# Optimization experiments

Measured on AMD Instinct MI355X. Metric: run time of the kernel, lower is better.

The kernel has to match this reference:

```python
import jax, jax.numpy as jnp
import numpy as np

DIM = 512
HEADS = 8
WS = 8  # window_size


def setup_inputs() -> dict:
    key = jax.random.key(0)
    ks = jax.random.split(key, 7)
    b, c, h, w = 4, DIM, 192, 192
    x = jax.random.normal(ks[0], (b, c, h, w), dtype=jnp.float32)
    # conv1x1 weights are [out, in] matrices (kernel dim squeezed)
    wq = jax.random.normal(ks[1], (DIM, DIM), dtype=jnp.float32) * 0.02
    wk = jax.random.normal(ks[2], (DIM, DIM), dtype=jnp.float32) * 0.02
    wv = jax.random.normal(ks[3], (DIM, DIM), dtype=jnp.float32) * 0.02
    wo = jax.random.normal(ks[4], (DIM, DIM), dtype=jnp.float32) * 0.02
    bo = jax.random.normal(ks[5], (DIM,), dtype=jnp.float32) * 0.02
    # learned per-head additive bias over window tokens (trunc_normal std=0.02)
    beta = jax.random.normal(ks[6], (HEADS, WS * WS, WS * WS), dtype=jnp.float32) * 0.02
    return {"x": x, "wq": wq, "wk": wk, "wv": wv, "wo": wo, "bo": bo, "beta": beta}


def reference(x, wq, wk, wv, wo, bo, beta):
    b, c, h, w = x.shape
    s = WS
    pad_r = (-w) % s
    pad_b = (-h) % s
    x = jnp.pad(x, ((0, 0), (0, 0), (0, pad_b), (0, pad_r)))
    H, W = h + pad_b, w + pad_r
    nh, nw = H // s, W // s
    n = s * s
    head_dim = c // HEADS
    scale = head_dim ** -0.5
    # window partition: (b, c, nh, s, nw, s) -> (b*nh*nw, c, n)
    xw = x.reshape(b, c, nh, s, nw, s).transpose(0, 2, 4, 1, 3, 5).reshape(b * nh * nw, c, n)
    B = xw.shape[0]
    q = jnp.einsum('oc,bcn->bon', wq, xw).reshape(B, HEADS, head_dim, n)
    k = jnp.einsum('oc,bcn->bon', wk, xw).reshape(B, HEADS, head_dim, n)
    v = jnp.einsum('oc,bcn->bon', wv, xw).reshape(B, HEADS, head_dim, n)
    attn = jnp.einsum('bhdn,bhdm->bhnm', q, k) * scale + beta  # [B,H,n,n]
    attn = jax.nn.softmax(attn, axis=-1)
    o = jnp.einsum('bhnm,bhdm->bhdn', attn, v).reshape(B, c, n)
    o = jnp.einsum('oc,bcn->bon', wo, o) + bo[None, :, None]
    # window merge back to image
    out = o.reshape(b, nh, nw, c, s, s).transpose(0, 3, 1, 4, 2, 5).reshape(b, c, H, W)
    return out[:, :, :h, :w]
```

## Files before the change

kernel.cpp:

```cpp
#include <hip/hip_runtime.h>

typedef unsigned short ushort_t;
typedef __attribute__((ext_vector_type(4))) float f32x4;
typedef __attribute__((ext_vector_type(8))) short short8;

__device__ __forceinline__ ushort_t f2bf(float f) {
  union { float f; unsigned u; } v; v.f = f;
  unsigned r = v.u + 0x7fffu + ((v.u >> 16) & 1u);
  return (ushort_t)(r >> 16);
}
__device__ __forceinline__ unsigned pack2(float lo, float hi) {
  return (unsigned)f2bf(lo) | ((unsigned)f2bf(hi) << 16);
}

__global__ __launch_bounds__(256) void cvt_w_k(const float* __restrict__ wq,
                                               const float* __restrict__ wk,
                                               const float* __restrict__ wv,
                                               const float* __restrict__ wo,
                                               ushort_t* __restrict__ dst) {
  int idx = (blockIdx.x * 256 + threadIdx.x) * 4;
  int m = idx >> 18;
  int off = idx & 0x3ffff;
  const float* s = (m == 0) ? wq : (m == 1) ? wk : (m == 2) ? wv : wo;
  float4 v = *(const float4*)(s + off);
  ushort4 o;
  o.x = f2bf(v.x); o.y = f2bf(v.y); o.z = f2bf(v.z); o.w = f2bf(v.w);
  *(ushort4*)(dst + idx) = o;
}

__global__ __launch_bounds__(256) void xpose_k(const float* __restrict__ x,
                                               ushort_t* __restrict__ xT) {
  __shared__ ushort_t tile[128 * 80];
  int bid = blockIdx.x;
  int win = bid >> 2, kc = bid & 3;
  int b = win / 576, rem = win % 576, wh = rem / 24, ww = rem % 24;
  int tid = threadIdx.x;
  {
    int c_l = tid >> 1, half = tid & 1;
    const float* xb = x + ((((size_t)b * 512 + kc * 128 + c_l) * 192 + wh * 8) * 192 + ww * 8);
#pragma unroll
    for (int ii = 0; ii < 4; ++ii) {
      int i = half * 4 + ii;
      float4 v0 = *(const float4*)(xb + i * 192);
      float4 v1 = *(const float4*)(xb + i * 192 + 4);
      uint4 u;
      u.x = (unsigned)f2bf(v0.x) | ((unsigned)f2bf(v0.y) << 16);
      u.y = (unsigned)f2bf(v0.z) | ((unsigned)f2bf(v0.w) << 16);
      u.z = (unsigned)f2bf(v1.x) | ((unsigned)f2bf(v1.y) << 16);
      u.w = (unsigned)f2bf(v1.z) | ((unsigned)f2bf(v1.w) << 16);
      *(uint4*)&tile[c_l * 80 + i * 8] = u;
    }
  }
  __syncthreads();
  {
    int tok = tid >> 2, q = tid & 3;
    unsigned w[16];
#pragma unroll
    for (int k = 0; k < 16; ++k) {
      unsigned lo = tile[(q * 32 + 2 * k) * 80 + tok];
      unsigned hi = tile[(q * 32 + 2 * k + 1) * 80 + tok];
      w[k] = lo | (hi << 16);
    }
    ushort_t* d = xT + ((size_t)(win * 64 + tok) * 512 + kc * 128 + q * 32);
#pragma unroll
    for (int s2 = 0; s2 < 4; ++s2) {
      uint4 u; u.x = w[s2 * 4 + 0]; u.y = w[s2 * 4 + 1]; u.z = w[s2 * 4 + 2]; u.w = w[s2 * 4 + 3];
      *(uint4*)(d + s2 * 8) = u;
    }
  }
}

__global__ __launch_bounds__(512, 2) void qkv_attn5_k(const ushort_t* __restrict__ xT,
                                                      const ushort_t* __restrict__ wB,
                                                      const float* __restrict__ beta,
                                                      ushort_t* __restrict__ O) {
  __shared__ __align__(16) ushort_t smem[2 * 8704 + 2 * 4608 + 2 * 4608];
  ushort_t* xstage = smem;
  ushort_t* qs = smem + 17408;
  ushort_t* ks = smem + 26624;
  ushort_t* vs = smem;

  int win = blockIdx.x;
  int t0 = win * 64;
  int tid = threadIdx.x, lane = tid & 63, wid = tid >> 6;
  int l15 = lane & 15, l4 = lane >> 4;

  int srow[2], sslot[2];
#pragma unroll
  for (int c = 0; c < 2; ++c) { int u = c * 512 + tid; srow[c] = u >> 4; sslot[c] = u & 15; }

  const f32x4 z = {0.f, 0.f, 0.f, 0.f};

  for (int hcc = 0; hcc < 4; ++hcc) {
    f32x4 aq[4], ak[4], av[4];
#pragma unroll
    for (int i = 0; i < 4; ++i) { aq[i] = z; ak[i] = z; av[i] = z; }
    int ocol = hcc * 128 + wid * 16 + l15;
    const ushort_t* wqr = wB + (size_t)ocol * 512 + l4 * 8;
    const ushort_t* wkr = wqr + 262144;
    const ushort_t* wvr = wqr + 524288;

#pragma unroll
    for (int c = 0; c < 2; ++c) {
      uint4 v = *(const uint4*)&xT[(size_t)(t0 + srow[c]) * 512 + sslot[c] * 8];
      *(uint4*)&xstage[srow[c] * 136 + sslot[c] * 8] = v;
    }
    __syncthreads();

#pragma unroll
    for (int kb = 0; kb < 4; ++kb) {
      uint4 nx[2];
      if (kb < 3) {
#pragma unroll
        for (int c = 0; c < 2; ++c)
          nx[c] = *(const uint4*)&xT[(size_t)(t0 + srow[c]) * 512 + (kb + 1) * 128 + sslot[c] * 8];
      }
      const ushort_t* xb = xstage + (kb & 1) * 8704;
      __builtin_amdgcn_s_setprio(1);
#pragma unroll
      for (int kkL = 0; kkL < 4; ++kkL) {
        int kk = kb * 4 + kkL;
        short8 bq = *(const short8*)(wqr + kk * 32);
        short8 bk = *(const short8*)(wkr + kk * 32);
        short8 bv = *(const short8*)(wvr + kk * 32);
#pragma unroll
        for (int nt = 0; nt < 4; ++nt) {
          short8 a = *(const short8*)&xb[(nt * 16 + l15) * 136 + kkL * 32 + l4 * 8];
          aq[nt] = __builtin_amdgcn_mfma_f32_16x16x32_bf16(a, bq, aq[nt], 0, 0, 0);
          ak[nt] = __builtin_amdgcn_mfma_f32_16x16x32_bf16(a, bk, ak[nt], 0, 0, 0);
          av[nt] = __builtin_amdgcn_mfma_f32_16x16x32_bf16(a, bv, av[nt], 0, 0, 0);
        }
      }
      __builtin_amdgcn_s_setprio(0);
      if (kb < 3) {
#pragma unroll
        for (int c = 0; c < 2; ++c)
          *(uint4*)&xstage[((kb + 1) & 1) * 8704 + srow[c] * 136 + sslot[c] * 8] = nx[c];
        __syncthreads();
      }
    }
    __syncthreads();

    int hw = wid >> 2;
    int dd = (wid * 16 + l15) & 63;
#pragma unroll
    for (int nt = 0; nt < 4; ++nt) {
#pragma unroll
      for (int r = 0; r < 4; ++r) {
        int n = nt * 16 + l4 * 4 + r;
        qs[hw * 4608 + n * 72 + dd] = f2bf(aq[nt][r]);
        ks[hw * 4608 + n * 72 + dd] = f2bf(ak[nt][r]);
      }
      uint2 u;
      u.x = pack2(av[nt][0], av[nt][1]);
      u.y = pack2(av[nt][2], av[nt][3]);
      *(uint2*)&vs[hw * 4608 + dd * 72 + nt * 16 + l4 * 4] = u;
    }
    __syncthreads();

    int hh = wid >> 2, rowg = wid & 3;
    int h = hcc * 2 + hh;
    f32x4 sA[4];
#pragma unroll
    for (int i = 0; i < 4; ++i) sA[i] = z;
#pragma unroll
    for (int kk = 0; kk < 2; ++kk) {
      short8 aF = *(const short8*)&qs[hh * 4608 + (rowg * 16 + l15) * 72 + kk * 32 + l4 * 8];
#pragma unroll
      for (int mt = 0; mt < 4; ++mt) {
        short8 bF = *(const short8*)&ks[hh * 4608 + (mt * 16 + l15) * 72 + kk * 32 + l4 * 8];
        sA[mt] = __builtin_amdgcn_mfma_f32_16x16x32_bf16(aF, bF, sA[mt], 0, 0, 0);
      }
    }
    const float* betah = beta + h * 4096;
    float p[4][4];
    float rmax[4] = {-1e30f, -1e30f, -1e30f, -1e30f};
#pragma unroll
    for (int mt = 0; mt < 4; ++mt)
#pragma unroll
      for (int r = 0; r < 4; ++r) {
        int n = rowg * 16 + l4 * 4 + r;
        float val = sA[mt][r] * 0.125f + betah[n * 64 + mt * 16 + l15];
        p[mt][r] = val;
        rmax[r] = fmaxf(rmax[r], val);
      }
#pragma unroll
    for (int m = 1; m <= 8; m <<= 1)
#pragma unroll
      for (int r = 0; r < 4; ++r) rmax[r] = fmaxf(rmax[r], __shfl_xor(rmax[r], m, 64));
    float rsum[4] = {0.f, 0.f, 0.f, 0.f};
#pragma unroll
    for (int mt = 0; mt < 4; ++mt)
#pragma unroll
      for (int r = 0; r < 4; ++r) {
        p[mt][r] = __expf(p[mt][r] - rmax[r]);
        rsum[r] += p[mt][r];
      }
#pragma unroll
    for (int m = 1; m <= 8; m <<= 1)
#pragma unroll
      for (int r = 0; r < 4; ++r) rsum[r] += __shfl_xor(rsum[r], m, 64);
    float rinv[4];
#pragma unroll
    for (int r = 0; r < 4; ++r) rinv[r] = 1.f / rsum[r];
#pragma unroll
    for (int mt = 0; mt < 4; ++mt)
#pragma unroll
      for (int r = 0; r < 4; ++r)
        qs[hh * 4608 + (rowg * 16 + l4 * 4 + r) * 72 + mt * 16 + l15] = f2bf(p[mt][r] * rinv[r]);

    f32x4 oA[4];
#pragma unroll
    for (int i = 0; i < 4; ++i) oA[i] = z;
#pragma unroll
    for (int kk = 0; kk < 2; ++kk) {
      short8 aF = *(const short8*)&qs[hh * 4608 + (rowg * 16 + l15) * 72 + kk * 32 + l4 * 8];
#pragma unroll
      for (int dt = 0; dt < 4; ++dt) {
        short8 bF = *(const short8*)&vs[hh * 4608 + (dt * 16 + l15) * 72 + kk * 32 + l4 * 8];
        oA[dt] = __builtin_amdgcn_mfma_f32_16x16x32_bf16(aF, bF, oA[dt], 0, 0, 0);
      }
    }
#pragma unroll
    for (int dt = 0; dt < 4; ++dt)
#pragma unroll
      for (int r = 0; r < 4; ++r) {
        int n = rowg * 16 + l4 * 4 + r;
        O[(size_t)(t0 + n) * 512 + h * 64 + dt * 16 + l15] = f2bf(oA[dt][r]);
      }
    __syncthreads();
  }
}

__global__ __launch_bounds__(256) void proj_kb(const ushort_t* __restrict__ O,
                                               const ushort_t* __restrict__ woB,
                                               const float* __restrict__ bo,
                                               float* __restrict__ out) {
  __shared__ ushort_t ows[64 * 136];
  int bid = blockIdx.x;
  int wg = (bid & 7) * 576 + (bid >> 3);
  int win = wg >> 1, mo = (wg & 1) * 256;
  int b = win / 576, rem = win % 576, wh = rem / 24, ww = rem % 24;
  int tid = threadIdx.x, lane = tid & 63, wid = tid >> 6;
  int l15 = lane & 15, l4 = lane >> 4;
  int t0 = win * 64;
  f32x4 z = {0.f, 0.f, 0.f, 0.f};
  f32x4 acc[4][4];
#pragma unroll
  for (int i = 0; i < 4; ++i)
#pragma unroll
    for (int j = 0; j < 4; ++j) acc[i][j] = z;
  int stok = tid >> 2, sq = tid & 3;
  for (int kcc = 0; kcc < 4; ++kcc) {
    {
      const uint4* src = (const uint4*)(O + ((size_t)(t0 + stok) * 512 + kcc * 128 + sq * 32));
      uint4* dstv = (uint4*)&ows[stok * 136 + sq * 32];
#pragma unroll
      for (int s2 = 0; s2 < 4; ++s2) dstv[s2] = src[s2];
    }
    __syncthreads();
#pragma unroll
    for (int kk = 0; kk < 4; ++kk) {
      short8 bF[4];
#pragma unroll
      for (int nt = 0; nt < 4; ++nt)
        bF[nt] = *(const short8*)&ows[(nt * 16 + l15) * 136 + kk * 32 + l4 * 8];
      int cg = kcc * 128 + kk * 32 + l4 * 8;
#pragma unroll
      for (int mt = 0; mt < 4; ++mt) {
        int orow = mo + wid * 64 + mt * 16 + l15;
        short8 aF = *(const short8*)(woB + (size_t)orow * 512 + cg);
#pragma unroll
        for (int nt = 0; nt < 4; ++nt)
          acc[mt][nt] = __builtin_amdgcn_mfma_f32_16x16x32_bf16(aF, bF[nt], acc[mt][nt], 0, 0, 0);
      }
    }
    __syncthreads();
  }
#pragma unroll
  for (int mt = 0; mt < 4; ++mt) {
#pragma unroll
    for (int r = 0; r < 4; ++r) {
      int o = mo + wid * 64 + mt * 16 + l4 * 4 + r;
      float bias = bo[o];
#pragma unroll
      for (int nt = 0; nt < 4; ++nt) {
        int tok = nt * 16 + l15;
        int i = tok >> 3, j = tok & 7;
        out[(((size_t)b * 512 + o) * 192 + wh * 8 + i) * 192 + ww * 8 + j] = acc[mt][nt][r] + bias;
      }
    }
  }
}

extern "C" void kernel_launch(void* const* d_in, const int* in_sizes, int n_in,
                              void* d_out, int out_size, void* d_ws, size_t ws_size,
                              hipStream_t stream) {
  const float* x    = (const float*)d_in[0];
  const float* wq   = (const float*)d_in[1];
  const float* wk   = (const float*)d_in[2];
  const float* wv   = (const float*)d_in[3];
  const float* wo   = (const float*)d_in[4];
  const float* bo   = (const float*)d_in[5];
  const float* beta = (const float*)d_in[6];

  ushort_t* wB = (ushort_t*)d_ws;
  ushort_t* xT = (ushort_t*)((char*)d_ws + (size_t)2097152);
  ushort_t* O  = (ushort_t*)((char*)d_ws + (size_t)2097152 + (size_t)147456 * 1024);

  cvt_w_k<<<1024, 256, 0, stream>>>(wq, wk, wv, wo, wB);
  xpose_k<<<2304 * 4, 256, 0, stream>>>(x, xT);
  qkv_attn5_k<<<2304, 512, 0, stream>>>(xT, wB, beta, O);
  proj_kb<<<4608, 256, 0, stream>>>(O, wB + 3 * 262144, bo, (float*)d_out);
}
```

Before: 858.5 us.

## Process two windows per QKV-attention block and full output channels per projection block

The fused QKV+attention kernel now handles 128 tokens (two windows) per block, so each weight fragment loaded from global memory feeds twice as many MFMAs. In exchange it uses more LDS and accumulators and drops occupancy to one block per SIMD group. Each head's attention then runs per window, with the two wave halves taking turns writing Q/K/V to shared memory. The projection kernel now computes all 512 output channels per window with 512 threads, so each O tile is staged once instead of twice, and block indices are swizzled across windows.

```diff
diff --git a/kernel.cpp b/kernel.cpp
--- a/kernel.cpp
+++ b/kernel.cpp
@@ -70,38 +70,39 @@
   }
 }
 
-__global__ __launch_bounds__(512, 2) void qkv_attn5_k(const ushort_t* __restrict__ xT,
+__global__ __launch_bounds__(512, 1) void qkv_attn6_k(const ushort_t* __restrict__ xT,
                                                       const ushort_t* __restrict__ wB,
                                                       const float* __restrict__ beta,
                                                       ushort_t* __restrict__ O) {
-  __shared__ __align__(16) ushort_t smem[2 * 8704 + 2 * 4608 + 2 * 4608];
+  __shared__ __align__(16) ushort_t smem[62464];
   ushort_t* xstage = smem;
-  ushort_t* qs = smem + 17408;
-  ushort_t* ks = smem + 26624;
-  ushort_t* vs = smem;
-
-  int win = blockIdx.x;
-  int t0 = win * 64;
+  ushort_t* qs = smem + 34816;
+  ushort_t* ks = smem + 44032;
+  ushort_t* vs = smem + 53248;
+
+  int bid = blockIdx.x;
+  int wg = (bid & 7) * 144 + (bid >> 3);
+  int t0 = wg * 128;
   int tid = threadIdx.x, lane = tid & 63, wid = tid >> 6;
   int l15 = lane & 15, l4 = lane >> 4;
 
-  int srow[2], sslot[2];
-#pragma unroll
-  for (int c = 0; c < 2; ++c) { int u = c * 512 + tid; srow[c] = u >> 4; sslot[c] = u & 15; }
+  int srow[4], sslot[4];
+#pragma unroll
+  for (int c = 0; c < 4; ++c) { int u = c * 512 + tid; srow[c] = u >> 4; sslot[c] = u & 15; }
 
   const f32x4 z = {0.f, 0.f, 0.f, 0.f};
 
   for (int hcc = 0; hcc < 4; ++hcc) {
-    f32x4 aq[4], ak[4], av[4];
-#pragma unroll
-    for (int i = 0; i < 4; ++i) { aq[i] = z; ak[i] = z; av[i] = z; }
+    f32x4 aq[8], ak[8], av[8];
+#pragma unroll
+    for (int i = 0; i < 8; ++i) { aq[i] = z; ak[i] = z; av[i] = z; }
     int ocol = hcc * 128 + wid * 16 + l15;
     const ushort_t* wqr = wB + (size_t)ocol * 512 + l4 * 8;
     const ushort_t* wkr = wqr + 262144;
     const ushort_t* wvr = wqr + 524288;
 
 #pragma unroll
-    for (int c = 0; c < 2; ++c) {
+    for (int c = 0; c < 4; ++c) {
       uint4 v = *(const uint4*)&xT[(size_t)(t0 + srow[c]) * 512 + sslot[c] * 8];
       *(uint4*)&xstage[srow[c] * 136 + sslot[c] * 8] = v;
     }
@@ -109,13 +110,13 @@
 
 #pragma unroll
     for (int kb = 0; kb < 4; ++kb) {
-      uint4 nx[2];
+      uint4 nx[4];
       if (kb < 3) {
 #pragma unroll
-        for (int c = 0; c < 2; ++c)
+        for (int c = 0; c < 4; ++c)
           nx[c] = *(const uint4*)&xT[(size_t)(t0 + srow[c]) * 512 + (kb + 1) * 128 + sslot[c] * 8];
       }
-      const ushort_t* xb = xstage + (kb & 1) * 8704;
+      const ushort_t* xb = xstage + (kb & 1) * 17408;
       __builtin_amdgcn_s_setprio(1);
 #pragma unroll
       for (int kkL = 0; kkL < 4; ++kkL) {
@@ -124,7 +125,7 @@
         short8 bk = *(const short8*)(wkr + kk * 32);
         short8 bv = *(const short8*)(wvr + kk * 32);
 #pragma unroll
-        for (int nt = 0; nt < 4; ++nt) {
+        for (int nt = 0; nt < 8; ++nt) {
           short8 a = *(const short8*)&xb[(nt * 16 + l15) * 136 + kkL * 32 + l4 * 8];
           aq[nt] = __builtin_amdgcn_mfma_f32_16x16x32_bf16(a, bq, aq[nt], 0, 0, 0);
           ak[nt] = __builtin_amdgcn_mfma_f32_16x16x32_bf16(a, bk, ak[nt], 0, 0, 0);
@@ -134,130 +135,137 @@
       __builtin_amdgcn_s_setprio(0);
       if (kb < 3) {
 #pragma unroll
-        for (int c = 0; c < 2; ++c)
-          *(uint4*)&xstage[((kb + 1) & 1) * 8704 + srow[c] * 136 + sslot[c] * 8] = nx[c];
+        for (int c = 0; c < 4; ++c)
+          *(uint4*)&xstage[((kb + 1) & 1) * 17408 + srow[c] * 136 + sslot[c] * 8] = nx[c];
         __syncthreads();
       }
     }
-    __syncthreads();
-
-    int hw = wid >> 2;
-    int dd = (wid * 16 + l15) & 63;
-#pragma unroll
-    for (int nt = 0; nt < 4; ++nt) {
-#pragma unroll
-      for (int r = 0; r < 4; ++r) {
-        int n = nt * 16 + l4 * 4 + r;
-        qs[hw * 4608 + n * 72 + dd] = f2bf(aq[nt][r]);
-        ks[hw * 4608 + n * 72 + dd] = f2bf(ak[nt][r]);
-      }
-      uint2 u;
-      u.x = pack2(av[nt][0], av[nt][1]);
-      u.y = pack2(av[nt][2], av[nt][3]);
-      *(uint2*)&vs[hw * 4608 + dd * 72 + nt * 16 + l4 * 4] = u;
-    }
-    __syncthreads();
-
-    int hh = wid >> 2, rowg = wid & 3;
-    int h = hcc * 2 + hh;
-    f32x4 sA[4];
-#pragma unroll
-    for (int i = 0; i < 4; ++i) sA[i] = z;
-#pragma unroll
-    for (int kk = 0; kk < 2; ++kk) {
-      short8 aF = *(const short8*)&qs[hh * 4608 + (rowg * 16 + l15) * 72 + kk * 32 + l4 * 8];
-#pragma unroll
-      for (int mt = 0; mt < 4; ++mt) {
-        short8 bF = *(const short8*)&ks[hh * 4608 + (mt * 16 + l15) * 72 + kk * 32 + l4 * 8];
-        sA[mt] = __builtin_amdgcn_mfma_f32_16x16x32_bf16(aF, bF, sA[mt], 0, 0, 0);
-      }
-    }
-    const float* betah = beta + h * 4096;
-    float p[4][4];
-    float rmax[4] = {-1e30f, -1e30f, -1e30f, -1e30f};
-#pragma unroll
-    for (int mt = 0; mt < 4; ++mt)
-#pragma unroll
-      for (int r = 0; r < 4; ++r) {
-        int n = rowg * 16 + l4 * 4 + r;
-        float val = sA[mt][r] * 0.125f + betah[n * 64 + mt * 16 + l15];
-        p[mt][r] = val;
-        rmax[r] = fmaxf(rmax[r], val);
-      }
-#pragma unroll
-    for (int m = 1; m <= 8; m <<= 1)
-#pragma unroll
-      for (int r = 0; r < 4; ++r) rmax[r] = fmaxf(rmax[r], __shfl_xor(rmax[r], m, 64));
-    float rsum[4] = {0.f, 0.f, 0.f, 0.f};
-#pragma unroll
-    for (int mt = 0; mt < 4; ++mt)
-#pragma unroll
-      for (int r = 0; r < 4; ++r) {
-        p[mt][r] = __expf(p[mt][r] - rmax[r]);
-        rsum[r] += p[mt][r];
-      }
-#pragma unroll
-    for (int m = 1; m <= 8; m <<= 1)
-#pragma unroll
-      for (int r = 0; r < 4; ++r) rsum[r] += __shfl_xor(rsum[r], m, 64);
-    float rinv[4];
-#pragma unroll
-    for (int r = 0; r < 4; ++r) rinv[r] = 1.f / rsum[r];
-#pragma unroll
-    for (int mt = 0; mt < 4; ++mt)
-#pragma unroll
-      for (int r = 0; r < 4; ++r)
-        qs[hh * 4608 + (rowg * 16 + l4 * 4 + r) * 72 + mt * 16 + l15] = f2bf(p[mt][r] * rinv[r]);
-
-    f32x4 oA[4];
-#pragma unroll
-    for (int i = 0; i < 4; ++i) oA[i] = z;
-#pragma unroll
-    for (int kk = 0; kk < 2; ++kk) {
-      short8 aF = *(const short8*)&qs[hh * 4608 + (rowg * 16 + l15) * 72 + kk * 32 + l4 * 8];
-#pragma unroll
-      for (int dt = 0; dt < 4; ++dt) {
-        short8 bF = *(const short8*)&vs[hh * 4608 + (dt * 16 + l15) * 72 + kk * 32 + l4 * 8];
-        oA[dt] = __builtin_amdgcn_mfma_f32_16x16x32_bf16(aF, bF, oA[dt], 0, 0, 0);
-      }
-    }
-#pragma unroll
-    for (int dt = 0; dt < 4; ++dt)
-#pragma unroll
-      for (int r = 0; r < 4; ++r) {
-        int n = rowg * 16 + l4 * 4 + r;
-        O[(size_t)(t0 + n) * 512 + h * 64 + dt * 16 + l15] = f2bf(oA[dt][r]);
-      }
-    __syncthreads();
-  }
-}
-
-__global__ __launch_bounds__(256) void proj_kb(const ushort_t* __restrict__ O,
-                                               const ushort_t* __restrict__ woB,
-                                               const float* __restrict__ bo,
-                                               float* __restrict__ out) {
+
+#pragma unroll
+    for (int s = 0; s < 2; ++s) {
+      __syncthreads();
+      if ((wid >> 2) == s) {
+        int dd = (wid * 16 + l15) & 63;
+#pragma unroll
+        for (int nt = 0; nt < 8; ++nt) {
+          int wn = nt >> 2, ntl = nt & 3;
+#pragma unroll
+          for (int r = 0; r < 4; ++r) {
+            int n = ntl * 16 + l4 * 4 + r;
+            qs[wn * 4608 + n * 72 + dd] = f2bf(aq[nt][r]);
+            ks[wn * 4608 + n * 72 + dd] = f2bf(ak[nt][r]);
+          }
+          uint2 u;
+          u.x = pack2(av[nt][0], av[nt][1]);
+          u.y = pack2(av[nt][2], av[nt][3]);
+          *(uint2*)&vs[wn * 4608 + dd * 72 + ntl * 16 + l4 * 4] = u;
+        }
+      }
+      __syncthreads();
+
+      int wn = wid >> 2, rowg = wid & 3;
+      int h = hcc * 2 + s;
+      f32x4 sA[4];
+#pragma unroll
+      for (int i = 0; i < 4; ++i) sA[i] = z;
+#pragma unroll
+      for (int kk = 0; kk < 2; ++kk) {
+        short8 aF = *(const short8*)&qs[wn * 4608 + (rowg * 16 + l15) * 72 + kk * 32 + l4 * 8];
+#pragma unroll
+        for (int mt = 0; mt < 4; ++mt) {
+          short8 bF = *(const short8*)&ks[wn * 4608 + (mt * 16 + l15) * 72 + kk * 32 + l4 * 8];
+          sA[mt] = __builtin_amdgcn_mfma_f32_16x16x32_bf16(aF, bF, sA[mt], 0, 0, 0);
+        }
+      }
+      const float* betah = beta + h * 4096;
+      float p[4][4];
+      float rmax[4] = {-1e30f, -1e30f, -1e30f, -1e30f};
+#pragma unroll
+      for (int mt = 0; mt < 4; ++mt)
+#pragma unroll
+        for (int r = 0; r < 4; ++r) {
+          int n = rowg * 16 + l4 * 4 + r;
+          float val = sA[mt][r] * 0.125f + betah[n * 64 + mt * 16 + l15];
+          p[mt][r] = val;
+          rmax[r] = fmaxf(rmax[r], val);
+        }
+#pragma unroll
+      for (int m = 1; m <= 8; m <<= 1)
+#pragma unroll
+        for (int r = 0; r < 4; ++r) rmax[r] = fmaxf(rmax[r], __shfl_xor(rmax[r], m, 64));
+      float rsum[4] = {0.f, 0.f, 0.f, 0.f};
+#pragma unroll
+      for (int mt = 0; mt < 4; ++mt)
+#pragma unroll
+        for (int r = 0; r < 4; ++r) {
+          p[mt][r] = __expf(p[mt][r] - rmax[r]);
+          rsum[r] += p[mt][r];
+        }
+#pragma unroll
+      for (int m = 1; m <= 8; m <<= 1)
+#pragma unroll
+        for (int r = 0; r < 4; ++r) rsum[r] += __shfl_xor(rsum[r], m, 64);
+      float rinv[4];
+#pragma unroll
+      for (int r = 0; r < 4; ++r) rinv[r] = 1.f / rsum[r];
+#pragma unroll
+      for (int mt = 0; mt < 4; ++mt)
+#pragma unroll
+        for (int r = 0; r < 4; ++r)
+          qs[wn * 4608 + (rowg * 16 + l4 * 4 + r) * 72 + mt * 16 + l15] = f2bf(p[mt][r] * rinv[r]);
+
+      f32x4 oA[4];
+#pragma unroll
+      for (int i = 0; i < 4; ++i) oA[i] = z;
+#pragma unroll
+      for (int kk = 0; kk < 2; ++kk) {
+        short8 aF = *(const short8*)&qs[wn * 4608 + (rowg * 16 + l15) * 72 + kk * 32 + l4 * 8];
+#pragma unroll
+        for (int dt = 0; dt < 4; ++dt) {
+          short8 bF = *(const short8*)&vs[wn * 4608 + (dt * 16 + l15) * 72 + kk * 32 + l4 * 8];
+          oA[dt] = __builtin_amdgcn_mfma_f32_16x16x32_bf16(aF, bF, oA[dt], 0, 0, 0);
+        }
+      }
+#pragma unroll
+      for (int dt = 0; dt < 4; ++dt)
+#pragma unroll
+        for (int r = 0; r < 4; ++r) {
+          int n = rowg * 16 + l4 * 4 + r;
+          O[(size_t)(t0 + wn * 64 + n) * 512 + h * 64 + dt * 16 + l15] = f2bf(oA[dt][r]);
+        }
+    }
+  }
+}
+
+__global__ __launch_bounds__(512, 2) void proj_kc(const ushort_t* __restrict__ O,
+                                                  const ushort_t* __restrict__ woB,
+                                                  const float* __restrict__ bo,
+                                                  float* __restrict__ out) {
   __shared__ ushort_t ows[64 * 136];
   int bid = blockIdx.x;
-  int wg = (bid & 7) * 576 + (bid >> 3);
-  int win = wg >> 1, mo = (wg & 1) * 256;
+  int win = (bid & 7) * 288 + (bid >> 3);
   int b = win / 576, rem = win % 576, wh = rem / 24, ww = rem % 24;
   int tid = threadIdx.x, lane = tid & 63, wid = tid >> 6;
   int l15 = lane & 15, l4 = lane >> 4;
   int t0 = win * 64;
-  f32x4 z = {0.f, 0.f, 0.f, 0.f};
+  const f32x4 z = {0.f, 0.f, 0.f, 0.f};
   f32x4 acc[4][4];
 #pragma unroll
   for (int i = 0; i < 4; ++i)
 #pragma unroll
     for (int j = 0; j < 4; ++j) acc[i][j] = z;
-  int stok = tid >> 2, sq = tid & 3;
+  int srow[2], sslot[2];
+#pragma unroll
+  for (int c = 0; c < 2; ++c) { int u = c * 512 + tid; srow[c] = u >> 4; sslot[c] = u & 15; }
   for (int kcc = 0; kcc < 4; ++kcc) {
-    {
-      const uint4* src = (const uint4*)(O + ((size_t)(t0 + stok) * 512 + kcc * 128 + sq * 32));
-      uint4* dstv = (uint4*)&ows[stok * 136 + sq * 32];
-#pragma unroll
-      for (int s2 = 0; s2 < 4; ++s2) dstv[s2] = src[s2];
-    }
+    uint4 t[2];
+#pragma unroll
+    for (int c = 0; c < 2; ++c)
+      t[c] = *(const uint4*)&O[(size_t)(t0 + srow[c]) * 512 + kcc * 128 + sslot[c] * 8];
+    __syncthreads();
+#pragma unroll
+    for (int c = 0; c < 2; ++c)
+      *(uint4*)&ows[srow[c] * 136 + sslot[c] * 8] = t[c];
     __syncthreads();
 #pragma unroll
     for (int kk = 0; kk < 4; ++kk) {
@@ -268,20 +276,19 @@
       int cg = kcc * 128 + kk * 32 + l4 * 8;
 #pragma unroll
       for (int mt = 0; mt < 4; ++mt) {
-        int orow = mo + wid * 64 + mt * 16 + l15;
+        int orow = wid * 64 + mt * 16 + l15;
         short8 aF = *(const short8*)(woB + (size_t)orow * 512 + cg);
 #pragma unroll
         for (int nt = 0; nt < 4; ++nt)
           acc[mt][nt] = __builtin_amdgcn_mfma_f32_16x16x32_bf16(aF, bF[nt], acc[mt][nt], 0, 0, 0);
       }
     }
-    __syncthreads();
   }
 #pragma unroll
   for (int mt = 0; mt < 4; ++mt) {
 #pragma unroll
     for (int r = 0; r < 4; ++r) {
-      int o = mo + wid * 64 + mt * 16 + l4 * 4 + r;
+      int o = wid * 64 + mt * 16 + l4 * 4 + r;
       float bias = bo[o];
 #pragma unroll
       for (int nt = 0; nt < 4; ++nt) {
@@ -310,6 +317,6 @@
 
   cvt_w_k<<<1024, 256, 0, stream>>>(wq, wk, wv, wo, wB);
   xpose_k<<<2304 * 4, 256, 0, stream>>>(x, xT);
-  qkv_attn5_k<<<2304, 512, 0, stream>>>(xT, wB, beta, O);
-  proj_kb<<<4608, 256, 0, stream>>>(O, wB + 3 * 262144, bo, (float*)d_out);
-}
+  qkv_attn6_k<<<1152, 512, 0, stream>>>(xT, wB, beta, O);
+  proj_kc<<<2304, 512, 0, stream>>>(O, wB + 3 * 262144, bo, (float*)d_out);
+}
```

Result: slower. 1.579 ms (+83.9%).

## Switch QKV projection to 32x32x16 MFMA tiles with 2D wave split

Applied to the files above, without the earlier changes.

The QKV projection inside the fused attention kernel now uses 32x32x16 bf16 MFMA instead of 16x16x32. Waves are split 4 ways over output columns and 2 ways over tokens, so each wave computes one 32x32 tile per matrix. That replaces 12 small MFMAs with 3 larger ones per k step and cuts LDS reads of the activation tile. The epilogue that writes Q/K/V to shared memory is remapped to the 32x32 accumulator layout. The weight loads from global become narrower per k step, and the larger accumulators add register pressure.

```diff
diff --git a/kernel.cpp b/kernel.cpp
--- a/kernel.cpp
+++ b/kernel.cpp
@@ -2,6 +2,7 @@
 
 typedef unsigned short ushort_t;
 typedef __attribute__((ext_vector_type(4))) float f32x4;
+typedef __attribute__((ext_vector_type(16))) float f32x16;
 typedef __attribute__((ext_vector_type(8))) short short8;
 
 __device__ __forceinline__ ushort_t f2bf(float f) {
@@ -70,10 +71,10 @@
   }
 }
 
-__global__ __launch_bounds__(512, 2) void qkv_attn5_k(const ushort_t* __restrict__ xT,
-                                                      const ushort_t* __restrict__ wB,
-                                                      const float* __restrict__ beta,
-                                                      ushort_t* __restrict__ O) {
+__global__ __launch_bounds__(512, 2) void qkv_attn32_k(const ushort_t* __restrict__ xT,
+                                                       const ushort_t* __restrict__ wB,
+                                                       const float* __restrict__ beta,
+                                                       ushort_t* __restrict__ O) {
   __shared__ __align__(16) ushort_t smem[2 * 8704 + 2 * 4608 + 2 * 4608];
   ushort_t* xstage = smem;
   ushort_t* qs = smem + 17408;
@@ -84,6 +85,8 @@
   int t0 = win * 64;
   int tid = threadIdx.x, lane = tid & 63, wid = tid >> 6;
   int l15 = lane & 15, l4 = lane >> 4;
+  int l31 = lane & 31, l5 = lane >> 5;
+  int cw = wid & 3, tw = wid >> 2;
 
   int srow[2], sslot[2];
 #pragma unroll
@@ -92,11 +95,11 @@
   const f32x4 z = {0.f, 0.f, 0.f, 0.f};
 
   for (int hcc = 0; hcc < 4; ++hcc) {
-    f32x4 aq[4], ak[4], av[4];
-#pragma unroll
-    for (int i = 0; i < 4; ++i) { aq[i] = z; ak[i] = z; av[i] = z; }
-    int ocol = hcc * 128 + wid * 16 + l15;
-    const ushort_t* wqr = wB + (size_t)ocol * 512 + l4 * 8;
+    f32x16 aq, ak, av;
+#pragma unroll
+    for (int i = 0; i < 16; ++i) { aq[i] = 0.f; ak[i] = 0.f; av[i] = 0.f; }
+    int ocol = hcc * 128 + cw * 32 + l31;
+    const ushort_t* wqr = wB + (size_t)ocol * 512 + l5 * 8;
     const ushort_t* wkr = wqr + 262144;
     const ushort_t* wvr = wqr + 524288;
 
@@ -118,18 +121,15 @@
       const ushort_t* xb = xstage + (kb & 1) * 8704;
       __builtin_amdgcn_s_setprio(1);
 #pragma unroll
-      for (int kkL = 0; kkL < 4; ++kkL) {
-        int kk = kb * 4 + kkL;
-        short8 bq = *(const short8*)(wqr + kk * 32);
-        short8 bk = *(const short8*)(wkr + kk * 32);
-        short8 bv = *(const short8*)(wvr + kk * 32);
-#pragma unroll
-        for (int nt = 0; nt < 4; ++nt) {
-          short8 a = *(const short8*)&xb[(nt * 16 + l15) * 136 + kkL * 32 + l4 * 8];
-          aq[nt] = __builtin_amdgcn_mfma_f32_16x16x32_bf16(a, bq, aq[nt], 0, 0, 0);
-          ak[nt] = __builtin_amdgcn_mfma_f32_16x16x32_bf16(a, bk, ak[nt], 0, 0, 0);
-          av[nt] = __builtin_amdgcn_mfma_f32_16x16x32_bf16(a, bv, av[nt], 0, 0, 0);
-        }
+      for (int kkL = 0; kkL < 8; ++kkL) {
+        int kk = kb * 8 + kkL;
+        short8 bq = *(const short8*)(wqr + kk * 16);
+        short8 bk = *(const short8*)(wkr + kk * 16);
+        short8 bv = *(const short8*)(wvr + kk * 16);
+        short8 a = *(const short8*)&xb[(tw * 32 + l31) * 136 + kkL * 16 + l5 * 8];
+        aq = __builtin_amdgcn_mfma_f32_32x32x16_bf16(a, bq, aq, 0, 0, 0);
+        ak = __builtin_amdgcn_mfma_f32_32x32x16_bf16(a, bk, ak, 0, 0, 0);
+        av = __builtin_amdgcn_mfma_f32_32x32x16_bf16(a, bv, av, 0, 0, 0);
       }
       __builtin_amdgcn_s_setprio(0);
       if (kb < 3) {
@@ -141,20 +141,21 @@
     }
     __syncthreads();
 
-    int hw = wid >> 2;
-    int dd = (wid * 16 + l15) & 63;
-#pragma unroll
-    for (int nt = 0; nt < 4; ++nt) {
-#pragma unroll
-      for (int r = 0; r < 4; ++r) {
-        int n = nt * 16 + l4 * 4 + r;
-        qs[hw * 4608 + n * 72 + dd] = f2bf(aq[nt][r]);
-        ks[hw * 4608 + n * 72 + dd] = f2bf(ak[nt][r]);
-      }
+    int hw = cw >> 1;
+    int dbase = (cw & 1) * 32 + l31;
+#pragma unroll
+    for (int reg = 0; reg < 16; ++reg) {
+      int m = tw * 32 + (reg & 3) + 8 * (reg >> 2) + 4 * l5;
+      qs[hw * 4608 + m * 72 + dbase] = f2bf(aq[reg]);
+      ks[hw * 4608 + m * 72 + dbase] = f2bf(ak[reg]);
+    }
+#pragma unroll
+    for (int g = 0; g < 4; ++g) {
+      int m0 = tw * 32 + 8 * g + 4 * l5;
       uint2 u;
-      u.x = pack2(av[nt][0], av[nt][1]);
-      u.y = pack2(av[nt][2], av[nt][3]);
-      *(uint2*)&vs[hw * 4608 + dd * 72 + nt * 16 + l4 * 4] = u;
+      u.x = pack2(av[g * 4 + 0], av[g * 4 + 1]);
+      u.y = pack2(av[g * 4 + 2], av[g * 4 + 3]);
+      *(uint2*)&vs[hw * 4608 + dbase * 72 + m0] = u;
     }
     __syncthreads();
 
@@ -310,6 +311,6 @@
 
   cvt_w_k<<<1024, 256, 0, stream>>>(wq, wk, wv, wo, wB);
   xpose_k<<<2304 * 4, 256, 0, stream>>>(x, xT);
-  qkv_attn5_k<<<2304, 512, 0, stream>>>(xT, wB, beta, O);
+  qkv_attn32_k<<<2304, 512, 0, stream>>>(xT, wB, beta, O);
   proj_kb<<<4608, 256, 0, stream>>>(O, wB + 3 * 262144, bo, (float*)d_out);
 }
```

After: 1.287 ms. 1.5x slower.
